# Kernel tuning notes

Hardware: AMD Instinct MI355X
Metric: run time of the kernel (lower is better)

Reference implementation:

```python
import jax, jax.numpy as jnp
import numpy as np

N = 100000       # nodes
E = 3200000      # edges (avg degree 32)
NFEAT = 512
NHID = 256
NCLASS = 64
K = 10
ALPHA = 0.1


def setup_inputs() -> dict:
    key = jax.random.key(0)
    ks = jax.random.split(key, 6)
    x = jax.random.normal(ks[0], (N, NFEAT), dtype=jnp.float32)
    edge_index = jax.random.randint(ks[1], (2, E), 0, N)
    W1 = jax.random.normal(ks[2], (NFEAT, NHID), dtype=jnp.float32) / np.float32(np.sqrt(NFEAT))
    b1 = jnp.zeros((NHID,), jnp.float32)
    W2 = jax.random.normal(ks[3], (NHID, NCLASS), dtype=jnp.float32) / np.float32(np.sqrt(NHID))
    b2 = jnp.zeros((NCLASS,), jnp.float32)
    # PPR init of the K+1 GPR coefficients: alpha*(1-alpha)^k, last = (1-alpha)^K
    kk = jnp.arange(K + 1, dtype=jnp.float32)
    temp = (ALPHA * (1.0 - ALPHA) ** kk).astype(jnp.float32)
    temp = temp.at[-1].set(np.float32((1.0 - ALPHA) ** K))
    return {"x": x, "edge_index": edge_index, "W1": W1, "b1": b1, "W2": W2, "b2": b2, "temp": temp}


def reference(x, edge_index, W1, b1, W2, b2, temp):
    # MLP (dropout is identity in eval mode)
    h = jax.nn.relu(x @ W1 + b1)          # [N, NHID]
    h = h @ W2 + b2                        # [N, NCLASS]

    # gcn_norm with self-loops: D^-1/2 (A+I) D^-1/2
    row, col = edge_index[0], edge_index[1]
    loops = jnp.arange(N, dtype=row.dtype)
    row = jnp.concatenate([row, loops])
    col = jnp.concatenate([col, loops])
    w = jnp.ones(row.shape[0], h.dtype)
    deg = jax.ops.segment_sum(w, col, num_segments=N)
    dis = jnp.where(deg > 0, jax.lax.rsqrt(deg), 0.0)
    norm = dis[row] * w * dis[col]         # [E+N]

    # K-hop GPR propagation: hidden = sum_k temp[k] * A_hat^k h
    hidden = h * temp[0]
    for k in range(K):
        h = jax.ops.segment_sum(norm[:, None] * h[row], col, num_segments=N)
        hidden = hidden + temp[k + 1] * h
    return jax.nn.log_softmax(hidden, axis=1)
```

## Files before the change

kernel.cpp:

```cpp
#include <hip/hip_runtime.h>
#include <math.h>

#define NFEAT 512
#define NHID  256
#define NCLS  64
#define KHOP  10
#define LDSTRIDE 56
#define NXCD 8
#define FCHUNK 8192

typedef __attribute__((ext_vector_type(8))) short short8;
typedef __attribute__((ext_vector_type(4))) float f32x4;

__device__ __forceinline__ unsigned short f2bf(float f) {
    unsigned u = __float_as_uint(f);
    u += 0x7FFFu + ((u >> 16) & 1u);
    return (unsigned short)(u >> 16);
}
__device__ __forceinline__ float bf2f(unsigned short h) {
    return __uint_as_float((unsigned)h << 16);
}

__global__ __launch_bounds__(256) void castT_kernel(const float* __restrict__ src,
                                                    unsigned short* __restrict__ dst,
                                                    int K, int N)
{
    int i = blockIdx.x * 256 + threadIdx.x;
    if (i < K * N) {
        int k = i / N, n = i % N;
        dst[(long)n * K + k] = f2bf(src[i]);
    }
}

__global__ __launch_bounds__(256) void mfma_gemm1_f32(
    const float* __restrict__ A, const unsigned short* __restrict__ BT,
    const float* __restrict__ bias, unsigned short* __restrict__ C, int M)
{
    __shared__ unsigned short As[64 * LDSTRIDE];
    __shared__ unsigned short Bs[256 * LDSTRIDE];
    const int tid = threadIdx.x;
    const int wave = tid >> 6, lane = tid & 63;
    const int quad = lane >> 4, l16 = lane & 15;
    const int m0 = blockIdx.x * 64;

    f32x4 acc[4][4] = {};
    const int srow = tid >> 2;
    const int schunk = (tid & 3) * 8;

    for (int k0 = 0; k0 < NFEAT; k0 += 32) {
        {
            int rg = m0 + srow;
            short8 v = {};
            if (rg < M) {
                const float* p = A + (long)rg * NFEAT + k0 + schunk;
                float4 f0 = *(const float4*)p;
                float4 f1 = *(const float4*)(p + 4);
                v[0] = (short)f2bf(f0.x); v[1] = (short)f2bf(f0.y);
                v[2] = (short)f2bf(f0.z); v[3] = (short)f2bf(f0.w);
                v[4] = (short)f2bf(f1.x); v[5] = (short)f2bf(f1.y);
                v[6] = (short)f2bf(f1.z); v[7] = (short)f2bf(f1.w);
            }
            *(short8*)(As + srow * LDSTRIDE + schunk) = v;
        }
        #pragma unroll
        for (int i = 0; i < 4; i++) {
            int r = srow + i * 64;
            short8 v = *(const short8*)(BT + (long)r * NFEAT + k0 + schunk);
            *(short8*)(Bs + r * LDSTRIDE + schunk) = v;
        }
        __syncthreads();
        short8 af[4], bfr[4];
        #pragma unroll
        for (int mi = 0; mi < 4; mi++)
            af[mi] = *(const short8*)(As + (mi*16 + l16) * LDSTRIDE + quad*8);
        #pragma unroll
        for (int nj = 0; nj < 4; nj++)
            bfr[nj] = *(const short8*)(Bs + (wave*64 + nj*16 + l16) * LDSTRIDE + quad*8);
        #pragma unroll
        for (int mi = 0; mi < 4; mi++)
            #pragma unroll
            for (int nj = 0; nj < 4; nj++)
                acc[mi][nj] = __builtin_amdgcn_mfma_f32_16x16x32_bf16(af[mi], bfr[nj], acc[mi][nj], 0, 0, 0);
        __syncthreads();
    }

    #pragma unroll
    for (int mi = 0; mi < 4; mi++)
        #pragma unroll
        for (int r = 0; r < 4; r++) {
            int row = m0 + mi*16 + quad*4 + r;
            if (row >= M) continue;
            #pragma unroll
            for (int nj = 0; nj < 4; nj++) {
                int col = wave*64 + nj*16 + l16;
                float v = acc[mi][nj][r] + bias[col];
                C[(long)row * NHID + col] = f2bf(fmaxf(v, 0.f));
            }
        }
}

__global__ __launch_bounds__(256) void mfma_gemm2(
    const unsigned short* __restrict__ A, const unsigned short* __restrict__ BT,
    const float* __restrict__ bias, unsigned short* __restrict__ S,
    float* __restrict__ hidden, const float* __restrict__ temp,
    const float* __restrict__ dis, int M)
{
    __shared__ unsigned short As[128 * LDSTRIDE];
    __shared__ unsigned short Bs[64 * LDSTRIDE];
    const int tid = threadIdx.x;
    const int wave = tid >> 6, lane = tid & 63;
    const int quad = lane >> 4, l16 = lane & 15;
    const int m0 = blockIdx.x * 128;
    const float t0 = temp[0];

    f32x4 acc[2][4] = {};
    const int srow = tid >> 2;
    const int schunk = (tid & 3) * 8;

    for (int k0 = 0; k0 < NHID; k0 += 32) {
        #pragma unroll
        for (int i = 0; i < 2; i++) {
            int r = srow + i * 64;
            int rg = m0 + r;
            short8 v = {};
            if (rg < M) v = *(const short8*)(A + (long)rg * NHID + k0 + schunk);
            *(short8*)(As + r * LDSTRIDE + schunk) = v;
        }
        {
            short8 v = *(const short8*)(BT + (long)srow * NHID + k0 + schunk);
            *(short8*)(Bs + srow * LDSTRIDE + schunk) = v;
        }
        __syncthreads();
        short8 af[2], bfr[4];
        #pragma unroll
        for (int mi = 0; mi < 2; mi++)
            af[mi] = *(const short8*)(As + (wave*32 + mi*16 + l16) * LDSTRIDE + quad*8);
        #pragma unroll
        for (int nj = 0; nj < 4; nj++)
            bfr[nj] = *(const short8*)(Bs + (nj*16 + l16) * LDSTRIDE + quad*8);
        #pragma unroll
        for (int mi = 0; mi < 2; mi++)
            #pragma unroll
            for (int nj = 0; nj < 4; nj++)
                acc[mi][nj] = __builtin_amdgcn_mfma_f32_16x16x32_bf16(af[mi], bfr[nj], acc[mi][nj], 0, 0, 0);
        __syncthreads();
    }

    #pragma unroll
    for (int mi = 0; mi < 2; mi++)
        #pragma unroll
        for (int r = 0; r < 4; r++) {
            int row = m0 + wave*32 + mi*16 + quad*4 + r;
            if (row >= M) continue;
            float dr = dis[row];
            #pragma unroll
            for (int nj = 0; nj < 4; nj++) {
                int col = nj*16 + l16;
                float v = acc[mi][nj][r] + bias[col];
                long idx = (long)row * NCLS + col;
                S[idx] = f2bf(dr * v);
                hidden[idx] = t0 * v;
            }
        }
}

__global__ void count_kernel(const int* __restrict__ ei, int E, int* __restrict__ cnt)
{
    int e = blockIdx.x * blockDim.x + threadIdx.x;
    if (e < E) atomicAdd(&cnt[ei[E + e]], 1);
}

__global__ void dis_kernel(const int* __restrict__ cnt, float* __restrict__ dis, int Nn)
{
    int v = blockIdx.x * blockDim.x + threadIdx.x;
    if (v < Nn) dis[v] = rsqrtf((float)(cnt[v] + 1));
}

__global__ __launch_bounds__(256) void bsum_kernel(const int* __restrict__ cnt, int n,
                                                   int* __restrict__ bsum)
{
    __shared__ int ws[4];
    int i = blockIdx.x * 256 + threadIdx.x;
    int v = (i < n) ? ((cnt[i] + 7) & ~7) : 0;
    #pragma unroll
    for (int off = 1; off < 64; off <<= 1) v += __shfl_xor(v, off);
    if ((threadIdx.x & 63) == 0) ws[threadIdx.x >> 6] = v;
    __syncthreads();
    if (threadIdx.x == 0) bsum[blockIdx.x] = ws[0] + ws[1] + ws[2] + ws[3];
}

__global__ __launch_bounds__(512) void bscan_kernel(int* __restrict__ bsum, int nb)
{
    __shared__ int buf[512];
    int i = threadIdx.x;
    int v = (i < nb) ? bsum[i] : 0;
    buf[i] = v;
    __syncthreads();
    for (int off = 1; off < 512; off <<= 1) {
        int t = (i >= off) ? buf[i - off] : 0;
        __syncthreads();
        buf[i] += t;
        __syncthreads();
    }
    if (i < nb) bsum[i] = buf[i] - v;
}

__global__ __launch_bounds__(256) void pscan_kernel(const int* __restrict__ cnt, int n,
                                                    const int* __restrict__ bsum,
                                                    int* __restrict__ ptr)
{
    __shared__ int buf[256];
    int i = blockIdx.x * 256 + threadIdx.x;
    int v = (i < n) ? ((cnt[i] + 7) & ~7) : 0;
    buf[threadIdx.x] = v;
    __syncthreads();
    for (int off = 1; off < 256; off <<= 1) {
        int t = (threadIdx.x >= off) ? buf[threadIdx.x - off] : 0;
        __syncthreads();
        buf[threadIdx.x] += t;
        __syncthreads();
    }
    if (i < n) ptr[i] = bsum[blockIdx.x] + buf[threadIdx.x] - v;
    if (i == n - 1) ptr[n] = bsum[blockIdx.x] + buf[threadIdx.x];
}

__global__ __launch_bounds__(256) void fill2_kernel(const int* __restrict__ ei, int E, int Nn,
                                                    const int* __restrict__ ptr,
                                                    int* __restrict__ fill,
                                                    int* __restrict__ adj)
{
    const int s     = blockIdx.x & (NXCD - 1);
    const int chunk = blockIdx.x >> 3;
    const int lo = (int)(((long)s * Nn) / NXCD);
    const int hi = (int)(((long)(s + 1) * Nn) / NXCD);
    const int base = chunk * FCHUNK;
    int lim = base + FCHUNK; if (lim > E) lim = E;
    const int* colp = ei + E;
    for (int e0 = base + threadIdx.x * 4; e0 < lim; e0 += 1024) {
        int4 c4 = *(const int4*)(colp + e0);
        int c;
        c = c4.x; if (c >= lo && c < hi) { int r = ei[e0];     int p = atomicAdd(&fill[c], 1); adj[ptr[c] + p] = r; }
        c = c4.y; if (c >= lo && c < hi) { int r = ei[e0 + 1]; int p = atomicAdd(&fill[c], 1); adj[ptr[c] + p] = r; }
        c = c4.z; if (c >= lo && c < hi) { int r = ei[e0 + 2]; int p = atomicAdd(&fill[c], 1); adj[ptr[c] + p] = r; }
        c = c4.w; if (c >= lo && c < hi) { int r = ei[e0 + 3]; int p = atomicAdd(&fill[c], 1); adj[ptr[c] + p] = r; }
    }
}

__global__ void padfill_kernel(const int* __restrict__ cnt, const int* __restrict__ ptr,
                               int* __restrict__ adj, int Nn)
{
    int v = blockIdx.x * 256 + threadIdx.x;
    if (v >= Nn) return;
    int b = ptr[v] + cnt[v], e = ptr[v + 1];
    for (int i = b; i < e; i++) adj[i] = Nn;
}

__global__ void zdum_kernel(unsigned short* __restrict__ sA,
                            unsigned short* __restrict__ sB, int Nn)
{
    int i = threadIdx.x;
    if (i < 64) sA[(long)Nn * NCLS + i] = 0;
    else        sB[(long)Nn * NCLS + (i - 64)] = 0;
}

__global__ __launch_bounds__(256) void prop_kernel(
    const unsigned short* __restrict__ sin, unsigned short* __restrict__ sout,
    float* __restrict__ hidden,
    const int* __restrict__ ptr, const int* __restrict__ adj,
    const float* __restrict__ dis, const float* __restrict__ temp, int k, int Nn)
{
    const int wave = threadIdx.x >> 6, lane = threadIdx.x & 63;
    const int v = blockIdx.x * 4 + wave;
    if (v >= Nn) return;

    const int beg = ptr[v], end = ptr[v + 1];
    const float d = dis[v];
    float acc = bf2f(sin[v * NCLS + lane]);

    for (int e = beg; e < end; e += 8) {
        int4 u0 = *(const int4*)(adj + e);
        int4 u1 = *(const int4*)(adj + e + 4);
        float a0 = bf2f(sin[u0.x * NCLS + lane]);
        float a1 = bf2f(sin[u0.y * NCLS + lane]);
        float a2 = bf2f(sin[u0.z * NCLS + lane]);
        float a3 = bf2f(sin[u0.w * NCLS + lane]);
        float a4 = bf2f(sin[u1.x * NCLS + lane]);
        float a5 = bf2f(sin[u1.y * NCLS + lane]);
        float a6 = bf2f(sin[u1.z * NCLS + lane]);
        float a7 = bf2f(sin[u1.w * NCLS + lane]);
        acc += ((a0 + a1) + (a2 + a3)) + ((a4 + a5) + (a6 + a7));
    }

    int idx = v * NCLS + lane;
    float h = d * acc;
    hidden[idx] += temp[k + 1] * h;
    sout[idx] = f2bf(d * h);
}

__global__ __launch_bounds__(256) void lsm_kernel(const float* __restrict__ hidden,
                                                  float* __restrict__ out, int Nn)
{
    const int wave = threadIdx.x >> 6, lane = threadIdx.x & 63;
    const int v = blockIdx.x * 4 + wave;
    if (v >= Nn) return;
    float x = hidden[(long)v * NCLS + lane];
    float m = x;
    #pragma unroll
    for (int off = 32; off > 0; off >>= 1) m = fmaxf(m, __shfl_xor(m, off));
    float s = __expf(x - m);
    #pragma unroll
    for (int off = 32; off > 0; off >>= 1) s += __shfl_xor(s, off);
    out[(long)v * NCLS + lane] = x - m - logf(s);
}

extern "C" void kernel_launch(void* const* d_in, const int* in_sizes, int n_in,
                              void* d_out, int out_size, void* d_ws, size_t ws_size,
                              hipStream_t stream)
{
    const float* x    = (const float*)d_in[0];
    const int*   ei   = (const int*)  d_in[1];
    const float* W1   = (const float*)d_in[2];
    const float* b1   = (const float*)d_in[3];
    const float* W2   = (const float*)d_in[4];
    const float* b2   = (const float*)d_in[5];
    const float* temp = (const float*)d_in[6];

    const int Nn = in_sizes[0] / NFEAT;
    const int E  = in_sizes[1] / 2;

    char* ws = (char*)d_ws;
    size_t off = 0;
    auto alloc = [&](size_t bytes) { size_t o = off; off += (bytes + 255) & ~255ull; return o; };

    size_t Epad = (size_t)E + 8ull * Nn;
    int*            adj    = (int*)           (ws + alloc(Epad * 4));
    unsigned short* sA     = (unsigned short*)(ws + alloc((size_t)(Nn + 1) * NCLS * 2));
    unsigned short* sB     = (unsigned short*)(ws + alloc((size_t)(Nn + 1) * NCLS * 2));
    float*          hidden = (float*)         (ws + alloc((size_t)Nn * NCLS * 4));
    unsigned short* hmid   = (unsigned short*)(ws + alloc((size_t)Nn * NHID * 2));
    unsigned short* W1T    = (unsigned short*)(ws + alloc((size_t)NFEAT * NHID * 2));
    unsigned short* W2T    = (unsigned short*)(ws + alloc((size_t)NHID * NCLS * 2));
    int*   cnt   = (int*)  (ws + alloc((size_t)Nn * 4));
    int*   fillb = (int*)  (ws + alloc((size_t)Nn * 4));
    float* dis   = (float*)(ws + alloc((size_t)Nn * 4));
    int*   ptr   = (int*)  (ws + alloc((size_t)(Nn + 1) * 4));
    int*   bsum  = (int*)  (ws + alloc(((size_t)Nn / 256 + 2) * 4));

    castT_kernel<<<(NFEAT * NHID + 255) / 256, 256, 0, stream>>>(W1, W1T, NFEAT, NHID);
    castT_kernel<<<(NHID * NCLS + 255) / 256, 256, 0, stream>>>(W2, W2T, NHID, NCLS);

    mfma_gemm1_f32<<<(Nn + 63) / 64, 256, 0, stream>>>(x, W1T, b1, hmid, Nn);

    hipMemsetAsync(cnt,   0, (size_t)Nn * 4, stream);
    hipMemsetAsync(fillb, 0, (size_t)Nn * 4, stream);
    count_kernel<<<(E + 255) / 256, 256, 0, stream>>>(ei, E, cnt);
    dis_kernel<<<(Nn + 255) / 256, 256, 0, stream>>>(cnt, dis, Nn);
    int nb = (Nn + 255) / 256;
    bsum_kernel<<<nb, 256, 0, stream>>>(cnt, Nn, bsum);
    bscan_kernel<<<1, 512, 0, stream>>>(bsum, nb);
    pscan_kernel<<<nb, 256, 0, stream>>>(cnt, Nn, bsum, ptr);
    int nch = (E + FCHUNK - 1) / FCHUNK;
    fill2_kernel<<<nch * NXCD, 256, 0, stream>>>(ei, E, Nn, ptr, fillb, adj);
    padfill_kernel<<<(Nn + 255) / 256, 256, 0, stream>>>(cnt, ptr, adj, Nn);
    zdum_kernel<<<1, 128, 0, stream>>>(sA, sB, Nn);

    mfma_gemm2<<<(Nn + 127) / 128, 256, 0, stream>>>(hmid, W2T, b2, sA, hidden, temp, dis, Nn);

    int pg = (Nn + 3) / 4;
    for (int k = 0; k < KHOP; k++) {
        const unsigned short* sin = (k & 1) ? sB : sA;
        unsigned short*       so  = (k & 1) ? sA : sB;
        prop_kernel<<<pg, 256, 0, stream>>>(sin, so, hidden, ptr, adj, dis, temp, k, Nn);
    }

    lsm_kernel<<<pg, 256, 0, stream>>>(hidden, (float*)d_out, Nn);
}
```

Baseline: 1.365 ms.

## Split propagation features into 16-column slabs pinned per XCD for L2 locality

Stores the propagated signal and the hidden accumulator as four column groups of 16 features each, laid out as separate slabs. Each XCD (chosen by blockIdx mod 8) handles one slab and half of the nodes, so a slab of about 3.2 MB fits in that XCD's L2 and neighbour gathers hit cache instead of HBM. Each wave now processes four edges in parallel with 16 lanes per edge and reduces with shuffles, and nontemporal hints are added on streaming loads and stores. The cost is that adjacency indices are read four times (once per slab), and each gathered row is only 32 bytes, which may lower coalescing efficiency.

New measurement: 4.066 ms. +197.8%, slower.

```diff
diff --git a/kernel.cpp b/kernel.cpp
--- a/kernel.cpp
+++ b/kernel.cpp
@@ -4,6 +4,7 @@
 #define NFEAT 512
 #define NHID  256
 #define NCLS  64
+#define NGRP  4
 #define KHOP  10
 #define LDSTRIDE 56
 #define NXCD 8
@@ -11,6 +12,7 @@
 
 typedef __attribute__((ext_vector_type(8))) short short8;
 typedef __attribute__((ext_vector_type(4))) float f32x4;
+typedef __attribute__((ext_vector_type(4))) int   i32x4;
 
 __device__ __forceinline__ unsigned short f2bf(float f) {
     unsigned u = __float_as_uint(f);
@@ -112,6 +114,7 @@
     const int quad = lane >> 4, l16 = lane & 15;
     const int m0 = blockIdx.x * 128;
     const float t0 = temp[0];
+    const long Np1 = (long)M + 1;
 
     f32x4 acc[2][4] = {};
     const int srow = tid >> 2;
@@ -155,11 +158,9 @@
             float dr = dis[row];
             #pragma unroll
             for (int nj = 0; nj < 4; nj++) {
-                int col = nj*16 + l16;
-                float v = acc[mi][nj][r] + bias[col];
-                long idx = (long)row * NCLS + col;
-                S[idx] = f2bf(dr * v);
-                hidden[idx] = t0 * v;
+                float v = acc[mi][nj][r] + bias[nj*16 + l16];
+                S[((long)nj * Np1 + row) * 16 + l16]      = f2bf(dr * v);
+                hidden[((long)nj * M + row) * 16 + l16]   = t0 * v;
             }
         }
 }
@@ -237,12 +238,12 @@
     int lim = base + FCHUNK; if (lim > E) lim = E;
     const int* colp = ei + E;
     for (int e0 = base + threadIdx.x * 4; e0 < lim; e0 += 1024) {
-        int4 c4 = *(const int4*)(colp + e0);
+        i32x4 c4 = __builtin_nontemporal_load((const i32x4*)(colp + e0));
         int c;
-        c = c4.x; if (c >= lo && c < hi) { int r = ei[e0];     int p = atomicAdd(&fill[c], 1); adj[ptr[c] + p] = r; }
-        c = c4.y; if (c >= lo && c < hi) { int r = ei[e0 + 1]; int p = atomicAdd(&fill[c], 1); adj[ptr[c] + p] = r; }
-        c = c4.z; if (c >= lo && c < hi) { int r = ei[e0 + 2]; int p = atomicAdd(&fill[c], 1); adj[ptr[c] + p] = r; }
-        c = c4.w; if (c >= lo && c < hi) { int r = ei[e0 + 3]; int p = atomicAdd(&fill[c], 1); adj[ptr[c] + p] = r; }
+        c = c4[0]; if (c >= lo && c < hi) { int r = __builtin_nontemporal_load(ei + e0);     int p = atomicAdd(&fill[c], 1); adj[ptr[c] + p] = r; }
+        c = c4[1]; if (c >= lo && c < hi) { int r = __builtin_nontemporal_load(ei + e0 + 1); int p = atomicAdd(&fill[c], 1); adj[ptr[c] + p] = r; }
+        c = c4[2]; if (c >= lo && c < hi) { int r = __builtin_nontemporal_load(ei + e0 + 2); int p = atomicAdd(&fill[c], 1); adj[ptr[c] + p] = r; }
+        c = c4[3]; if (c >= lo && c < hi) { int r = __builtin_nontemporal_load(ei + e0 + 3); int p = atomicAdd(&fill[c], 1); adj[ptr[c] + p] = r; }
     }
 }
 
@@ -259,51 +260,62 @@
                             unsigned short* __restrict__ sB, int Nn)
 {
     int i = threadIdx.x;
-    if (i < 64) sA[(long)Nn * NCLS + i] = 0;
-    else        sB[(long)Nn * NCLS + (i - 64)] = 0;
-}
-
-__global__ __launch_bounds__(256) void prop_kernel(
+    int g = (i & 63) >> 4, c = i & 15;
+    size_t idx = ((size_t)g * (Nn + 1) + Nn) * 16 + c;
+    if (i < 64) sA[idx] = 0;
+    else        sB[idx] = 0;
+}
+
+__global__ __launch_bounds__(256) void prop2_kernel(
     const unsigned short* __restrict__ sin, unsigned short* __restrict__ sout,
     float* __restrict__ hidden,
     const int* __restrict__ ptr, const int* __restrict__ adj,
-    const float* __restrict__ dis, const float* __restrict__ temp, int k, int Nn)
+    const float* __restrict__ dis, const float* __restrict__ temp,
+    int k, int Nn, int half)
+{
+    const int wave = threadIdx.x >> 6, lane = threadIdx.x & 63;
+    const int ns = lane >> 4, c = lane & 15;
+    const int xcd = blockIdx.x & 7;
+    const int g = xcd >> 1, sub = xcd & 1;
+    const int lb = blockIdx.x >> 3;
+
+    const int v0 = sub * half;
+    int vend = v0 + half; if (vend > Nn) vend = Nn;
+    const int v = v0 + lb * 4 + wave;
+    if (v >= vend) return;
+
+    const size_t slab = (size_t)g * (Nn + 1) * 16;
+    const unsigned short* sg = sin + slab;
+    unsigned short* og = sout + slab;
+    float* hg = hidden + (size_t)g * Nn * 16;
+
+    const int beg = ptr[v], end = ptr[v + 1];
+    const float d = dis[v];
+    float acc = (ns == 0) ? bf2f(sg[(size_t)v * 16 + c]) : 0.f;
+
+    for (int e = beg + ns; e < end; e += 4) {
+        int u = __builtin_nontemporal_load(adj + e);
+        acc += bf2f(sg[(size_t)u * 16 + c]);
+    }
+    acc += __shfl_xor(acc, 16);
+    acc += __shfl_xor(acc, 32);
+
+    if (ns == 0) {
+        float h = d * acc;
+        size_t idx = (size_t)v * 16 + c;
+        float hv = __builtin_nontemporal_load(hg + idx);
+        __builtin_nontemporal_store(hv + temp[k + 1] * h, hg + idx);
+        og[idx] = f2bf(d * h);
+    }
+}
+
+__global__ __launch_bounds__(256) void lsm_kernel(const float* __restrict__ hidden,
+                                                  float* __restrict__ out, int Nn)
 {
     const int wave = threadIdx.x >> 6, lane = threadIdx.x & 63;
     const int v = blockIdx.x * 4 + wave;
     if (v >= Nn) return;
-
-    const int beg = ptr[v], end = ptr[v + 1];
-    const float d = dis[v];
-    float acc = bf2f(sin[v * NCLS + lane]);
-
-    for (int e = beg; e < end; e += 8) {
-        int4 u0 = *(const int4*)(adj + e);
-        int4 u1 = *(const int4*)(adj + e + 4);
-        float a0 = bf2f(sin[u0.x * NCLS + lane]);
-        float a1 = bf2f(sin[u0.y * NCLS + lane]);
-        float a2 = bf2f(sin[u0.z * NCLS + lane]);
-        float a3 = bf2f(sin[u0.w * NCLS + lane]);
-        float a4 = bf2f(sin[u1.x * NCLS + lane]);
-        float a5 = bf2f(sin[u1.y * NCLS + lane]);
-        float a6 = bf2f(sin[u1.z * NCLS + lane]);
-        float a7 = bf2f(sin[u1.w * NCLS + lane]);
-        acc += ((a0 + a1) + (a2 + a3)) + ((a4 + a5) + (a6 + a7));
-    }
-
-    int idx = v * NCLS + lane;
-    float h = d * acc;
-    hidden[idx] += temp[k + 1] * h;
-    sout[idx] = f2bf(d * h);
-}
-
-__global__ __launch_bounds__(256) void lsm_kernel(const float* __restrict__ hidden,
-                                                  float* __restrict__ out, int Nn)
-{
-    const int wave = threadIdx.x >> 6, lane = threadIdx.x & 63;
-    const int v = blockIdx.x * 4 + wave;
-    if (v >= Nn) return;
-    float x = hidden[(long)v * NCLS + lane];
+    float x = hidden[((long)(lane >> 4) * Nn + v) * 16 + (lane & 15)];
     float m = x;
     #pragma unroll
     for (int off = 32; off > 0; off >>= 1) m = fmaxf(m, __shfl_xor(m, off));
@@ -366,12 +378,14 @@
 
     mfma_gemm2<<<(Nn + 127) / 128, 256, 0, stream>>>(hmid, W2T, b2, sA, hidden, temp, dis, Nn);
 
-    int pg = (Nn + 3) / 4;
+    int half = (Nn + 1) / 2;
+    int nbsub = (half + 3) / 4;
     for (int k = 0; k < KHOP; k++) {
         const unsigned short* sin = (k & 1) ? sB : sA;
         unsigned short*       so  = (k & 1) ? sA : sB;
-        prop_kernel<<<pg, 256, 0, stream>>>(sin, so, hidden, ptr, adj, dis, temp, k, Nn);
-    }
-
+        prop2_kernel<<<nbsub * NXCD, 256, 0, stream>>>(sin, so, hidden, ptr, adj, dis, temp, k, Nn, half);
+    }
+
+    int pg = (Nn + 3) / 4;
     lsm_kernel<<<pg, 256, 0, stream>>>(hidden, (float*)d_out, Nn);
 }
```
